# Kernel optimization log

Measured on AMD Instinct MI355X. Metric: run time of the kernel, lower is better.

Reference implementation:

```python
import jax, jax.numpy as jnp
import numpy as np

EMB = 128
HID = 128
N = 1024


def setup_inputs() -> dict:
    key = jax.random.key(0)
    ks = jax.random.split(key, 10)
    s1 = 1.0 / np.sqrt(2 * EMB)
    s2 = 1.0 / np.sqrt(HID)
    return {
        "z1": jax.random.normal(ks[0], (N, EMB), jnp.float32),
        "z2": jax.random.normal(ks[1], (N, EMB), jnp.float32),
        "W1": jax.random.uniform(ks[2], (HID, 2 * EMB), jnp.float32, -s1, s1),
        "b1": jax.random.uniform(ks[3], (HID,), jnp.float32, -s1, s1),
        "W2": jax.random.uniform(ks[4], (HID, HID), jnp.float32, -s2, s2),
        "b2": jax.random.uniform(ks[5], (HID,), jnp.float32, -s2, s2),
        "W3": jax.random.uniform(ks[6], (1, HID), jnp.float32, -s2, s2),
        "b3": jax.random.uniform(ks[7], (1,), jnp.float32, -s2, s2),
    }


def reference(z1, z2, W1, b1, W2, b2, W3, b3):
    # pairs[i, j] = concat(z1[j], z2[i]); first Linear split into two matmuls
    # so the [n, n, 2*emb] concat tensor is never materialized (same math).
    W1a = W1[:, :EMB]   # acts on z1 half
    W1b = W1[:, EMB:]   # acts on z2 half
    a = jnp.einsum('jd,hd->jh', z1, W1a)          # [n, h], varies along j
    b = jnp.einsum('id,hd->ih', z2, W1b)          # [n, h], varies along i
    h1 = jax.nn.gelu(a[None, :, :] + b[:, None, :] + b1, approximate=False)  # [n, n, h]
    h2 = jax.nn.gelu(jnp.einsum('ijh,gh->ijg', h1, W2) + b2, approximate=False)
    log_q = jnp.einsum('ijh,oh->ijo', h2, W3) + b3  # [n, n, 1]
    return log_q[..., 0]
```

## Files before the change

kernel.cpp:

```cpp
#include <hip/hip_runtime.h>

#define NN  1024
#define EMB 128
#define HID 128

typedef __attribute__((ext_vector_type(4))) float float4v;
typedef __attribute__((ext_vector_type(8))) short short8;

__device__ __forceinline__ float4v gelu4(float4v x) {
  float4v x2 = x * x;
  float4v t = x2 * 0.1029432f + 2.3022086f;
  float4v y = x * t;
  float4v e;
  e[0] = __builtin_amdgcn_exp2f(y[0]);
  e[1] = __builtin_amdgcn_exp2f(y[1]);
  e[2] = __builtin_amdgcn_exp2f(y[2]);
  e[3] = __builtin_amdgcn_exp2f(y[3]);
  float4v d = e + 1.0f;
  float4v rv;
  rv[0] = __builtin_amdgcn_rcpf(d[0]);
  rv[1] = __builtin_amdgcn_rcpf(d[1]);
  rv[2] = __builtin_amdgcn_rcpf(d[2]);
  rv[3] = __builtin_amdgcn_rcpf(d[3]);
  return x - x * rv;
}

__device__ __forceinline__ short bfrh(float g) {
  return (short)((__float_as_uint(g) + 0x8000u) >> 16);
}

__global__ __launch_bounds__(256)
void prep_kernel(const float* __restrict__ z1, const float* __restrict__ z2,
                 const float* __restrict__ W1, const float* __restrict__ b1,
                 const float* __restrict__ W2,
                 float* __restrict__ Abuf, float* __restrict__ Bbuf,
                 unsigned short* __restrict__ W2f) {
  int blk = blockIdx.x;
  int tid = threadIdx.x;
  if (blk < 128) {
    int which = blk >> 6;
    int j0 = (blk & 63) << 4;
    const float* z = which ? z2 : z1;
    int w = tid >> 6, l = tid & 63, r = l & 15, q = l >> 4;

    const float* zrow = z + (j0 + r) * EMB;
    const float* w1r0 = W1 + (w * 32 + r) * (2 * EMB) + which * EMB;
    const float* w1r1 = w1r0 + 16 * (2 * EMB);

    float4v acc[2] = {};
#pragma unroll
    for (int kt = 0; kt < 4; ++kt) {
      int k0 = kt * 32 + q * 8;
      float4v za = *(const float4v*)(zrow + k0);
      float4v zb = *(const float4v*)(zrow + k0 + 4);
      float4v wa0 = *(const float4v*)(w1r0 + k0);
      float4v wb0 = *(const float4v*)(w1r0 + k0 + 4);
      float4v wa1 = *(const float4v*)(w1r1 + k0);
      float4v wb1 = *(const float4v*)(w1r1 + k0 + 4);
      short8 az, b0f, b1f;
#pragma unroll
      for (int j = 0; j < 4; ++j) {
        az[j] = bfrh(za[j]);  az[j + 4] = bfrh(zb[j]);
        b0f[j] = bfrh(wa0[j]); b0f[j + 4] = bfrh(wb0[j]);
        b1f[j] = bfrh(wa1[j]); b1f[j + 4] = bfrh(wb1[j]);
      }
      acc[0] = __builtin_amdgcn_mfma_f32_16x16x32_bf16(az, b0f, acc[0], 0, 0, 0);
      acc[1] = __builtin_amdgcn_mfma_f32_16x16x32_bf16(az, b1f, acc[1], 0, 0, 0);
    }
    float ba0 = which ? 0.0f : b1[w * 32 + r];
    float ba1 = which ? 0.0f : b1[w * 32 + 16 + r];
    float* dst = which ? Bbuf : Abuf;
#pragma unroll
    for (int reg = 0; reg < 4; ++reg) {
      int row = j0 + q * 4 + reg;
      dst[row * HID + w * 32 + r]      = acc[0][reg] + ba0;
      dst[row * HID + w * 32 + 16 + r] = acc[1][reg] + ba1;
    }
  } else {
    int idx = (blk - 128) * 2048 + tid * 8;
    int lane = (idx >> 3) & 63;
    int nt = (idx >> 9) & 7;
    int kt = idx >> 12;
    int g = nt * 16 + (lane & 15);
    int hb = kt * 32 + (lane >> 4) * 8;
#pragma unroll
    for (int j = 0; j < 8; ++j) {
      unsigned u = __float_as_uint(W2[g * HID + hb + j]);
      W2f[idx + j] = (unsigned short)((u + 0x7FFFu + ((u >> 16) & 1u)) >> 16);
    }
  }
}

__global__ __launch_bounds__(256, 4)
void fused_mlp_kernel(const float* __restrict__ Abuf, const float* __restrict__ Bbuf,
                      const float* __restrict__ W2f4,
                      const float* __restrict__ b2, const float* __restrict__ W3,
                      const float* __restrict__ b3, float* __restrict__ out) {
  __shared__ __align__(16) short s_w2[HID * HID];

  int tid = threadIdx.x;
  {
    const float4v* src = (const float4v*)W2f4;
    float4v* dst = (float4v*)s_w2;
#pragma unroll
    for (int t = 0; t < 8; ++t)
      dst[tid + t * 256] = src[tid + t * 256];
  }

  int w = tid >> 6;
  int l = tid & 63;
  int r = l & 15;
  int q = l >> 4;

  int bi = (blockIdx.x >> 6) << 3;
  int bj = (blockIdx.x & 63) << 4;

  const float* Arow = Abuf + (bj + r) * HID;
  const float* B0 = Bbuf + (bi + w * 2) * HID;
  const float* B1 = B0 + HID;

  float4v acc[2][8] = {};

  __syncthreads();

#pragma unroll
  for (int kt = 0; kt < 4; ++kt) {
    int h0 = kt * 32 + q * 8;
    float4v a0 = *(const float4v*)(Arow + h0);
    float4v a1 = *(const float4v*)(Arow + h0 + 4);

    float4v g00 = gelu4(a0 + *(const float4v*)(B0 + h0));
    float4v g01 = gelu4(a1 + *(const float4v*)(B0 + h0 + 4));
    float4v g10 = gelu4(a0 + *(const float4v*)(B1 + h0));
    float4v g11 = gelu4(a1 + *(const float4v*)(B1 + h0 + 4));
    short8 af0, af1;
#pragma unroll
    for (int j = 0; j < 4; ++j) {
      af0[j] = bfrh(g00[j]); af0[j + 4] = bfrh(g01[j]);
      af1[j] = bfrh(g10[j]); af1[j + 4] = bfrh(g11[j]);
    }

    const short8* wrow = (const short8*)s_w2 + kt * 8 * 64 + l;
#pragma unroll
    for (int nt = 0; nt < 8; ++nt) {
      short8 bfr = wrow[nt * 64];
      acc[0][nt] = __builtin_amdgcn_mfma_f32_16x16x32_bf16(af0, bfr, acc[0][nt], 0, 0, 0);
      acc[1][nt] = __builtin_amdgcn_mfma_f32_16x16x32_bf16(af1, bfr, acc[1][nt], 0, 0, 0);
    }
  }

  float b2v[8], w3v[8];
#pragma unroll
  for (int nt = 0; nt < 8; ++nt) {
    b2v[nt] = b2[nt * 16 + r];
    w3v[nt] = W3[nt * 16 + r];
  }
  float bias3 = b3[0];

#pragma unroll
  for (int mt = 0; mt < 2; ++mt) {
    float4v s = {0.f, 0.f, 0.f, 0.f};
#pragma unroll
    for (int nt = 0; nt < 8; ++nt) {
      float4v xx = acc[mt][nt] + b2v[nt];
      s = s + gelu4(xx) * w3v[nt];
    }
#pragma unroll
    for (int mask = 1; mask < 16; mask <<= 1) {
#pragma unroll
      for (int reg = 0; reg < 4; ++reg)
        s[reg] += __shfl_xor(s[reg], mask, 64);
    }
    if (r < 4) {
      int irow = bi + w * 2 + mt;
      int jcol = bj + q * 4 + r;
      out[irow * NN + jcol] = s[r] + bias3;
    }
  }
}

extern "C" void kernel_launch(void* const* d_in, const int* in_sizes, int n_in,
                              void* d_out, int out_size, void* d_ws, size_t ws_size,
                              hipStream_t stream) {
  const float* z1 = (const float*)d_in[0];
  const float* z2 = (const float*)d_in[1];
  const float* W1 = (const float*)d_in[2];
  const float* b1 = (const float*)d_in[3];
  const float* W2 = (const float*)d_in[4];
  const float* b2 = (const float*)d_in[5];
  const float* W3 = (const float*)d_in[6];
  const float* b3 = (const float*)d_in[7];
  float* out = (float*)d_out;

  float* Abuf = (float*)d_ws;
  float* Bbuf = Abuf + NN * HID;
  unsigned short* W2f = (unsigned short*)(Bbuf + NN * HID);

  prep_kernel<<<136, 256, 0, stream>>>(z1, z2, W1, b1, W2, Abuf, Bbuf, W2f);
  fused_mlp_kernel<<<(NN / 8) * (NN / 16), 256, 0, stream>>>(
      Abuf, Bbuf, (const float*)W2f, b2, W3, b3, out);
}
```

Measured before the change: 159.5 us.

## Persist fused MLP blocks, batch GELU reciprocals, stage prep operands in LDS

The fused MLP kernel is now persistent. It launches 1024 blocks that each load W2 into LDS once and loop over 8 tiles, instead of 8192 blocks that each reload W2. GELU replaces four reciprocals with one shared reciprocal plus extra multiplies, and bf16 packing uses vector conversions. The prep kernel stages z and W1 in LDS in MFMA fragment layout before its MFMAs. The shared reciprocal of a product of four terms could overflow for large inputs.

```diff
diff --git a/kernel.cpp b/kernel.cpp
--- a/kernel.cpp
+++ b/kernel.cpp
@@ -5,7 +5,21 @@
 #define HID 128
 
 typedef __attribute__((ext_vector_type(4))) float float4v;
+typedef __attribute__((ext_vector_type(8))) float float8v;
 typedef __attribute__((ext_vector_type(8))) short short8;
+typedef __attribute__((ext_vector_type(4))) __bf16 bf16x4;
+typedef __attribute__((ext_vector_type(8))) __bf16 bf16x8;
+
+__device__ __forceinline__ short8 to_bf16x8(float4v a, float4v b) {
+  float8v f = {a[0], a[1], a[2], a[3], b[0], b[1], b[2], b[3]};
+  bf16x8 r = __builtin_convertvector(f, bf16x8);
+  return __builtin_bit_cast(short8, r);
+}
+
+__device__ __forceinline__ void store_bf16x4(short* p, float4v v) {
+  bf16x4 r = __builtin_convertvector(v, bf16x4);
+  *(bf16x4*)p = r;
+}
 
 __device__ __forceinline__ float4v gelu4(float4v x) {
   float4v x2 = x * x;
@@ -17,16 +31,21 @@
   e[2] = __builtin_amdgcn_exp2f(y[2]);
   e[3] = __builtin_amdgcn_exp2f(y[3]);
   float4v d = e + 1.0f;
+  float p01 = d[0] * d[1];
+  float p23 = d[2] * d[3];
+  float rall = __builtin_amdgcn_rcpf(p01 * p23);
+  float r01 = p23 * rall;
+  float r23 = p01 * rall;
   float4v rv;
-  rv[0] = __builtin_amdgcn_rcpf(d[0]);
-  rv[1] = __builtin_amdgcn_rcpf(d[1]);
-  rv[2] = __builtin_amdgcn_rcpf(d[2]);
-  rv[3] = __builtin_amdgcn_rcpf(d[3]);
+  rv[0] = d[1] * r01;
+  rv[1] = d[0] * r01;
+  rv[2] = d[3] * r23;
+  rv[3] = d[2] * r23;
   return x - x * rv;
 }
 
-__device__ __forceinline__ short bfrh(float g) {
-  return (short)((__float_as_uint(g) + 0x8000u) >> 16);
+__device__ __forceinline__ float4v mfma16(short8 a, short8 b, float4v c) {
+  return __builtin_amdgcn_mfma_f32_16x16x32_bf16(a, b, c, 0, 0, 0);
 }
 
 __global__ __launch_bounds__(256)
@@ -35,46 +54,58 @@
                  const float* __restrict__ W2,
                  float* __restrict__ Abuf, float* __restrict__ Bbuf,
                  unsigned short* __restrict__ W2f) {
-  int blk = blockIdx.x;
-  int tid = threadIdx.x;
+  int blk = blockIdx.x, tid = threadIdx.x;
   if (blk < 128) {
     int which = blk >> 6;
     int j0 = (blk & 63) << 4;
     const float* z = which ? z2 : z1;
+    __shared__ __align__(16) short zf[4 * 64 * 8];
+    __shared__ __align__(16) short w1f[HID * HID];
+
+    {
+      int row = tid >> 4;
+      int col = (tid & 15) * 8;
+      const float* zp = z + (j0 + row) * EMB + col;
+      float4v v0 = *(const float4v*)zp;
+      float4v v1 = *(const float4v*)(zp + 4);
+      int kt = col >> 5;
+      int lane = ((col >> 3) & 3) * 16 + row;
+      *(short8*)(zf + (kt * 64 + lane) * 8) = to_bf16x8(v0, v1);
+    }
+    {
+      const float* wbase = W1 + which * EMB;
+#pragma unroll
+      for (int p = 0; p < 16; ++p) {
+        int u = p * 256 + tid;
+        int g = u >> 5;
+        int c = (u & 31) * 4;
+        float4v v = *(const float4v*)(wbase + g * (2 * EMB) + c);
+        int kt = c >> 5;
+        int nt = g >> 4;
+        int lane = ((c >> 3) & 3) * 16 + (g & 15);
+        store_bf16x4(w1f + ((kt * 8 + nt) * 64 + lane) * 8 + (c & 7), v);
+      }
+    }
+    __syncthreads();
+
     int w = tid >> 6, l = tid & 63, r = l & 15, q = l >> 4;
-
-    const float* zrow = z + (j0 + r) * EMB;
-    const float* w1r0 = W1 + (w * 32 + r) * (2 * EMB) + which * EMB;
-    const float* w1r1 = w1r0 + 16 * (2 * EMB);
-
-    float4v acc[2] = {};
+    float4v acc0 = {}, acc1 = {};
 #pragma unroll
     for (int kt = 0; kt < 4; ++kt) {
-      int k0 = kt * 32 + q * 8;
-      float4v za = *(const float4v*)(zrow + k0);
-      float4v zb = *(const float4v*)(zrow + k0 + 4);
-      float4v wa0 = *(const float4v*)(w1r0 + k0);
-      float4v wb0 = *(const float4v*)(w1r0 + k0 + 4);
-      float4v wa1 = *(const float4v*)(w1r1 + k0);
-      float4v wb1 = *(const float4v*)(w1r1 + k0 + 4);
-      short8 az, b0f, b1f;
-#pragma unroll
-      for (int j = 0; j < 4; ++j) {
-        az[j] = bfrh(za[j]);  az[j + 4] = bfrh(zb[j]);
-        b0f[j] = bfrh(wa0[j]); b0f[j + 4] = bfrh(wb0[j]);
-        b1f[j] = bfrh(wa1[j]); b1f[j + 4] = bfrh(wb1[j]);
-      }
-      acc[0] = __builtin_amdgcn_mfma_f32_16x16x32_bf16(az, b0f, acc[0], 0, 0, 0);
-      acc[1] = __builtin_amdgcn_mfma_f32_16x16x32_bf16(az, b1f, acc[1], 0, 0, 0);
+      short8 az  = *(const short8*)(zf + (kt * 64 + l) * 8);
+      short8 bf0 = *(const short8*)(w1f + ((kt * 8 + w * 2) * 64 + l) * 8);
+      short8 bf1 = *(const short8*)(w1f + ((kt * 8 + w * 2 + 1) * 64 + l) * 8);
+      acc0 = mfma16(az, bf0, acc0);
+      acc1 = mfma16(az, bf1, acc1);
     }
     float ba0 = which ? 0.0f : b1[w * 32 + r];
     float ba1 = which ? 0.0f : b1[w * 32 + 16 + r];
-    float* dst = which ? Bbuf : Abuf;
+    float* dstp = which ? Bbuf : Abuf;
 #pragma unroll
     for (int reg = 0; reg < 4; ++reg) {
       int row = j0 + q * 4 + reg;
-      dst[row * HID + w * 32 + r]      = acc[0][reg] + ba0;
-      dst[row * HID + w * 32 + 16 + r] = acc[1][reg] + ba1;
+      dstp[row * HID + w * 32 + r]      = acc0[reg] + ba0;
+      dstp[row * HID + w * 32 + 16 + r] = acc1[reg] + ba1;
     }
   } else {
     int idx = (blk - 128) * 2048 + tid * 8;
@@ -107,47 +138,7 @@
       dst[tid + t * 256] = src[tid + t * 256];
   }
 
-  int w = tid >> 6;
-  int l = tid & 63;
-  int r = l & 15;
-  int q = l >> 4;
-
-  int bi = (blockIdx.x >> 6) << 3;
-  int bj = (blockIdx.x & 63) << 4;
-
-  const float* Arow = Abuf + (bj + r) * HID;
-  const float* B0 = Bbuf + (bi + w * 2) * HID;
-  const float* B1 = B0 + HID;
-
-  float4v acc[2][8] = {};
-
-  __syncthreads();
-
-#pragma unroll
-  for (int kt = 0; kt < 4; ++kt) {
-    int h0 = kt * 32 + q * 8;
-    float4v a0 = *(const float4v*)(Arow + h0);
-    float4v a1 = *(const float4v*)(Arow + h0 + 4);
-
-    float4v g00 = gelu4(a0 + *(const float4v*)(B0 + h0));
-    float4v g01 = gelu4(a1 + *(const float4v*)(B0 + h0 + 4));
-    float4v g10 = gelu4(a0 + *(const float4v*)(B1 + h0));
-    float4v g11 = gelu4(a1 + *(const float4v*)(B1 + h0 + 4));
-    short8 af0, af1;
-#pragma unroll
-    for (int j = 0; j < 4; ++j) {
-      af0[j] = bfrh(g00[j]); af0[j + 4] = bfrh(g01[j]);
-      af1[j] = bfrh(g10[j]); af1[j + 4] = bfrh(g11[j]);
-    }
-
-    const short8* wrow = (const short8*)s_w2 + kt * 8 * 64 + l;
-#pragma unroll
-    for (int nt = 0; nt < 8; ++nt) {
-      short8 bfr = wrow[nt * 64];
-      acc[0][nt] = __builtin_amdgcn_mfma_f32_16x16x32_bf16(af0, bfr, acc[0][nt], 0, 0, 0);
-      acc[1][nt] = __builtin_amdgcn_mfma_f32_16x16x32_bf16(af1, bfr, acc[1][nt], 0, 0, 0);
-    }
-  }
+  int w = tid >> 6, l = tid & 63, r = l & 15, q = l >> 4;
 
   float b2v[8], w3v[8];
 #pragma unroll
@@ -157,24 +148,59 @@
   }
   float bias3 = b3[0];
 
-#pragma unroll
-  for (int mt = 0; mt < 2; ++mt) {
-    float4v s = {0.f, 0.f, 0.f, 0.f};
-#pragma unroll
-    for (int nt = 0; nt < 8; ++nt) {
-      float4v xx = acc[mt][nt] + b2v[nt];
-      s = s + gelu4(xx) * w3v[nt];
-    }
-#pragma unroll
-    for (int mask = 1; mask < 16; mask <<= 1) {
-#pragma unroll
-      for (int reg = 0; reg < 4; ++reg)
-        s[reg] += __shfl_xor(s[reg], mask, 64);
-    }
-    if (r < 4) {
-      int irow = bi + w * 2 + mt;
-      int jcol = bj + q * 4 + r;
-      out[irow * NN + jcol] = s[r] + bias3;
+  int bj = (blockIdx.x & 63) << 4;
+  const float* Arow = Abuf + (bj + r) * HID;
+
+  __syncthreads();
+
+  for (int t = blockIdx.x; t < 64 * 128; t += 1024) {
+    int bi = (t >> 6) << 3;
+    const float* B0 = Bbuf + (bi + w * 2) * HID;
+    const float* B1 = B0 + HID;
+
+    float4v acc[2][8] = {};
+
+#pragma unroll
+    for (int kt = 0; kt < 4; ++kt) {
+      int h0 = kt * 32 + q * 8;
+      float4v a0 = *(const float4v*)(Arow + h0);
+      float4v a1 = *(const float4v*)(Arow + h0 + 4);
+
+      float4v g00 = gelu4(a0 + *(const float4v*)(B0 + h0));
+      float4v g01 = gelu4(a1 + *(const float4v*)(B0 + h0 + 4));
+      float4v g10 = gelu4(a0 + *(const float4v*)(B1 + h0));
+      float4v g11 = gelu4(a1 + *(const float4v*)(B1 + h0 + 4));
+      short8 af0 = to_bf16x8(g00, g01);
+      short8 af1 = to_bf16x8(g10, g11);
+
+      const short8* wrow = (const short8*)s_w2 + kt * 8 * 64 + l;
+#pragma unroll
+      for (int nt = 0; nt < 8; ++nt) {
+        short8 bfr = wrow[nt * 64];
+        acc[0][nt] = mfma16(af0, bfr, acc[0][nt]);
+        acc[1][nt] = mfma16(af1, bfr, acc[1][nt]);
+      }
+    }
+
+#pragma unroll
+    for (int mt = 0; mt < 2; ++mt) {
+      float4v s = {0.f, 0.f, 0.f, 0.f};
+#pragma unroll
+      for (int nt = 0; nt < 8; ++nt) {
+        float4v xx = acc[mt][nt] + b2v[nt];
+        s = s + gelu4(xx) * w3v[nt];
+      }
+#pragma unroll
+      for (int mask = 1; mask < 16; mask <<= 1) {
+#pragma unroll
+        for (int reg = 0; reg < 4; ++reg)
+          s[reg] += __shfl_xor(s[reg], mask, 64);
+      }
+      if (r < 4) {
+        int irow = bi + w * 2 + mt;
+        int jcol = bj + q * 4 + r;
+        out[irow * NN + jcol] = s[r] + bias3;
+      }
     }
   }
 }
@@ -197,6 +223,6 @@
   unsigned short* W2f = (unsigned short*)(Bbuf + NN * HID);
 
   prep_kernel<<<136, 256, 0, stream>>>(z1, z2, W1, b1, W2, Abuf, Bbuf, W2f);
-  fused_mlp_kernel<<<(NN / 8) * (NN / 16), 256, 0, stream>>>(
+  fused_mlp_kernel<<<1024, 256, 0, stream>>>(
       Abuf, Bbuf, (const float*)W2f, b2, W3, b3, out);
 }
```

Result: slower. 596.1 us (+273.7%).
